# Kernel tuning notes

Measured on AMD Instinct MI355X. Metric: run time of the kernel, lower is better.

## Reference

```python
import jax, jax.numpy as jnp
import numpy as np

D = 1024
N = 16
H = D // N  # 64
F = 4096
LOG2E = 1.442695041


def _rms_norm(x, scale, eps=1e-6):
    var = jnp.mean(x * x, axis=-1, keepdims=True)
    return x * jax.lax.rsqrt(var + eps) * scale


def _layer_norm(x, gamma, beta, eps=1e-5):
    m = jnp.mean(x, axis=-1, keepdims=True)
    v = jnp.mean(jnp.square(x - m), axis=-1, keepdims=True)
    return (x - m) * jax.lax.rsqrt(v + eps) * gamma + beta


def setup_inputs() -> dict:
    key = jax.random.key(0)
    ks = jax.random.split(key, 12)
    B, T = 8, 1024
    s = 0.02
    return {
        "x": jax.random.normal(ks[0], (B, T, D), dtype=jnp.float32),
        "padding": jnp.ones((B, T), dtype=jnp.float32),
        "rms_scale": jnp.ones((D,), dtype=jnp.float32),
        "per_dim_scale": jnp.zeros((H,), dtype=jnp.float32),
        "wq": jax.random.normal(ks[1], (D, N, H), dtype=jnp.float32) * s,
        "bq": jnp.zeros((N, H), dtype=jnp.float32),
        "wk": jax.random.normal(ks[2], (D, N, H), dtype=jnp.float32) * s,
        "bk": jnp.zeros((N, H), dtype=jnp.float32),
        "wv": jax.random.normal(ks[3], (D, N, H), dtype=jnp.float32) * s,
        "bv": jnp.zeros((N, H), dtype=jnp.float32),
        "wo": jax.random.normal(ks[4], (D, N, H), dtype=jnp.float32) * s,
        "bo": jnp.zeros((D,), dtype=jnp.float32),
        "ln_gamma": jnp.ones((D,), dtype=jnp.float32),
        "ln_beta": jnp.zeros((D,), dtype=jnp.float32),
        "w1": jax.random.normal(ks[5], (D, F), dtype=jnp.float32) * s,
        "b1": jnp.zeros((F,), dtype=jnp.float32),
        "w2": jax.random.normal(ks[6], (F, D), dtype=jnp.float32) * s,
        "b2": jnp.zeros((D,), dtype=jnp.float32),
    }


def reference(x, padding, rms_scale, per_dim_scale, wq, bq, wk, bk, wv, bv,
              wo, bo, ln_gamma, ln_beta, w1, b1, w2, b2):
    B, T, _ = x.shape
    res = x
    # pre-norm (RMS) for attention block
    xn = _rms_norm(x, rms_scale)
    # causal + padding mask: [B, T, S]
    causal = jnp.tril(jnp.ones((T, T), dtype=x.dtype))
    mask = causal[None, :, :] * padding[:, :, None] * padding[:, None, :]
    # projections: [B,T,N,H]
    q = jnp.einsum("btd,dnh->btnh", xn, wq) + bq
    k = jnp.einsum("btd,dnh->btnh", xn, wk) + bk
    v = jnp.einsum("btd,dnh->btnh", xn, wv) + bv
    # per-dim scale: (log2(e)/sqrt(H)) * softplus(p)
    scale = (LOG2E / jnp.sqrt(jnp.asarray(H, x.dtype))) * jax.nn.softplus(per_dim_scale)
    q = q * scale
    # scores: [B,N,T,S]
    dot = jnp.einsum("btnh,bsnh->bnts", q, k)
    dot = jnp.where(mask[:, None, :, :] == 0, jnp.asarray(-1e9, dot.dtype), dot)
    attn_w = jax.nn.softmax(dot, axis=-1)
    attn_out = jnp.einsum("bnts,bsnh->btnh", attn_w, v)
    attn = jnp.einsum("btnh,dnh->btd", attn_out, wo) + bo
    attn = res + attn
    # FFN block (pre-norm LayerNorm)
    res2 = attn
    h = _layer_norm(attn, ln_gamma, ln_beta)
    h = jax.nn.relu(h @ w1 + b1)
    h = h @ w2 + b2
    return res2 + h
```

## Files before the change

kernel.cpp:

```cpp
#include <hip/hip_runtime.h>
#include <hip/hip_bf16.h>
#include <cstdint>
#include <cstddef>

#define BB    8
#define TT    1024
#define DD    1024
#define NHEAD 16
#define HDIM  64
#define FF    4096

typedef unsigned short u16;
typedef unsigned int   u32;
typedef short bf16x8 __attribute__((ext_vector_type(8)));
typedef float floatx4 __attribute__((ext_vector_type(4)));
typedef float floatx16 __attribute__((ext_vector_type(16)));
typedef __attribute__((address_space(1))) const u32 gu32;
typedef __attribute__((address_space(3))) u32 lu32;

#define ZERO16 {0.f,0.f,0.f,0.f,0.f,0.f,0.f,0.f,0.f,0.f,0.f,0.f,0.f,0.f,0.f,0.f}

__device__ __forceinline__ float b2f(u16 u) {
  union { u32 i; float f; } c; c.i = ((u32)u) << 16; return c.f;
}
__device__ __forceinline__ u16 f2b(float f) {
  union { float f; u32 i; } c; c.f = f;
  u32 x = c.i;
  u32 r = (x + 0x7fffu + ((x >> 16) & 1u)) >> 16;
  return (u16)r;
}

__global__ __launch_bounds__(256) void rms_kernel(const float* __restrict__ x,
                                                  const float* __restrict__ g,
                                                  u16* __restrict__ xn) {
  int row = blockIdx.x;
  int tid = threadIdx.x;
  float4 v = ((const float4*)(x + (size_t)row * DD))[tid];
  float ss = v.x*v.x + v.y*v.y + v.z*v.z + v.w*v.w;
  for (int off = 32; off; off >>= 1) ss += __shfl_xor(ss, off);
  __shared__ float red[4];
  if ((tid & 63) == 0) red[tid >> 6] = ss;
  __syncthreads();
  float tot = red[0] + red[1] + red[2] + red[3];
  float inv = rsqrtf(tot * (1.0f / DD) + 1e-6f);
  float4 gv = ((const float4*)g)[tid];
  ushort4 o;
  o.x = f2b(v.x * inv * gv.x);
  o.y = f2b(v.y * inv * gv.y);
  o.z = f2b(v.z * inv * gv.z);
  o.w = f2b(v.w * inv * gv.w);
  ((ushort4*)(xn + (size_t)row * DD))[tid] = o;
}

__global__ __launch_bounds__(256) void ln_kernel(const float* __restrict__ a,
                                                 const float* __restrict__ g,
                                                 const float* __restrict__ be,
                                                 u16* __restrict__ o) {
  int row = blockIdx.x;
  int tid = threadIdx.x;
  float4 v = ((const float4*)(a + (size_t)row * DD))[tid];
  float s1 = v.x + v.y + v.z + v.w;
  float s2 = v.x*v.x + v.y*v.y + v.z*v.z + v.w*v.w;
  for (int off = 32; off; off >>= 1) {
    s1 += __shfl_xor(s1, off);
    s2 += __shfl_xor(s2, off);
  }
  __shared__ float r1[4], r2[4];
  if ((tid & 63) == 0) { r1[tid >> 6] = s1; r2[tid >> 6] = s2; }
  __syncthreads();
  float S1 = r1[0] + r1[1] + r1[2] + r1[3];
  float S2 = r2[0] + r2[1] + r2[2] + r2[3];
  float mean = S1 * (1.0f / DD);
  float var  = S2 * (1.0f / DD) - mean * mean;
  float inv  = rsqrtf(var + 1e-5f);
  float4 gv = ((const float4*)g)[tid];
  float4 bv = ((const float4*)be)[tid];
  ushort4 out;
  out.x = f2b((v.x - mean) * inv * gv.x + bv.x);
  out.y = f2b((v.y - mean) * inv * gv.y + bv.y);
  out.z = f2b((v.z - mean) * inv * gv.z + bv.z);
  out.w = f2b((v.w - mean) * inv * gv.w + bv.w);
  ((ushort4*)(o + (size_t)row * DD))[tid] = out;
}

__global__ void prep_kernel(const float* __restrict__ bq, const float* __restrict__ bk,
                            const float* __restrict__ bv, const float* __restrict__ pds,
                            float* __restrict__ bqkv, float* __restrict__ qsall) {
  int j = blockIdx.x * 1024 + threadIdx.x;
  float b = (j < 1024) ? bq[j] : (j < 2048) ? bk[j - 1024] : bv[j - 2048];
  bqkv[j] = b;
  float s = 1.f;
  if (j < 1024) {
    float p = pds[j & 63];
    float sp = (p > 0.f) ? (p + log1pf(__expf(-p))) : log1pf(__expf(p));
    s = 0.26017112252f * sp;
  }
  qsall[j] = s;
}

__global__ __launch_bounds__(256) void transpose_conv(const float* __restrict__ in,
                                                      u16* __restrict__ out,
                                                      int R, int C) {
  __shared__ float t[32][33];
  int bx = blockIdx.x * 32, by = blockIdx.y * 32;
  int tx = threadIdx.x & 31, ty = threadIdx.x >> 5;
#pragma unroll
  for (int i = 0; i < 32; i += 8)
    t[ty + i][tx] = in[(size_t)(by + ty + i) * C + bx + tx];
  __syncthreads();
#pragma unroll
  for (int i = 0; i < 32; i += 8)
    out[(size_t)(bx + ty + i) * R + by + tx] = f2b(t[tx][ty + i]);
}

__global__ __launch_bounds__(256) void conv_bf16(const float* __restrict__ in,
                                                 u16* __restrict__ out) {
  int i = blockIdx.x * 256 + threadIdx.x;
  float4 v = ((const float4*)in)[i];
  ushort4 o = { f2b(v.x), f2b(v.y), f2b(v.z), f2b(v.w) };
  ((ushort4*)out)[i] = o;
}

__global__ __launch_bounds__(256) void vtrans_kernel(const u16* __restrict__ vsrc,
                                                     u16* __restrict__ vdst) {
  __shared__ u16 tile[64][65];
  int bn = blockIdx.y; int b = bn >> 4, n = bn & 15;
  int t0 = blockIdx.x * 64;
  int tid = threadIdx.x;
  int rr = tid >> 4;
  int c4 = (tid & 15) * 4;
#pragma unroll
  for (int i = 0; i < 4; i++) {
    int r = i * 16 + rr;
    ushort4 d = *(const ushort4*)(vsrc + ((size_t)(b * TT + t0 + r)) * DD + n * HDIM + c4);
    tile[r][c4 + 0] = d.x; tile[r][c4 + 1] = d.y;
    tile[r][c4 + 2] = d.z; tile[r][c4 + 3] = d.w;
  }
  __syncthreads();
#pragma unroll
  for (int i = 0; i < 4; i++) {
    int h = i * 16 + rr;
    ushort4 d;
    d.x = tile[c4 + 0][h]; d.y = tile[c4 + 1][h];
    d.z = tile[c4 + 2][h]; d.w = tile[c4 + 3][h];
    *(ushort4*)(vdst + ((size_t)bn * HDIM + h) * TT + t0 + c4) = d;
  }
}

template <typename OUT_T>
__global__ __launch_bounds__(256) void mfma_gemm(
    const u16* __restrict__ A, const u16* __restrict__ Bt,
    const float* __restrict__ bias, const float* __restrict__ accsrc,
    const float* __restrict__ scale, OUT_T* __restrict__ C,
    int lda, int ldb, int K, int relu, int ldc, size_t regstride) {
  __shared__ u16 As[128 * 32] __attribute__((aligned(16)));
  __shared__ u16 Bs[128 * 32] __attribute__((aligned(16)));
  int tid = threadIdx.x;
  int lane = tid & 63;
  int wave = tid >> 6;
  int nbx = gridDim.x;
  int nwg = nbx * gridDim.y;
  int bid = blockIdx.y * nbx + blockIdx.x;
  int wid = (bid & 7) * (nwg >> 3) + (bid >> 3);
  int row0 = (wid / nbx) * 128, col0 = (wid % nbx) * 128;

  int sr = tid >> 2;
  int sk = (tid & 3) << 3;
  const u16* ag = A  + (size_t)(row0 + sr) * lda + sk;
  const u16* bg = Bt + (size_t)(col0 + sr) * ldb + sk;
  u16* asl = As + tid * 8;
  u16* bsl = Bs + tid * 8;
  size_t rstepA = (size_t)64 * lda;
  size_t rstepB = (size_t)64 * ldb;

  int wr = (wave >> 1) * 64;
  int wc = (wave & 1) * 64;
  int fr = lane & 15;
  int fq = lane >> 4;

  const bf16x8* afp = (const bf16x8*)(As + (size_t)(wr + fr) * 32 + fq * 8);
  const bf16x8* bfp = (const bf16x8*)(Bs + (size_t)(wc + fr) * 32 + fq * 8);

  floatx4 acc[4][4];
#pragma unroll
  for (int mi = 0; mi < 4; mi++)
#pragma unroll
    for (int ni = 0; ni < 4; ni++)
      acc[mi][ni] = (floatx4){0.f, 0.f, 0.f, 0.f};

  for (int k0 = 0; k0 < K; k0 += 32) {
    __builtin_amdgcn_global_load_lds((gu32*)ag,            (lu32*)asl,          16, 0, 0);
    __builtin_amdgcn_global_load_lds((gu32*)(ag + rstepA), (lu32*)(asl + 2048), 16, 0, 0);
    __builtin_amdgcn_global_load_lds((gu32*)bg,            (lu32*)bsl,          16, 0, 0);
    __builtin_amdgcn_global_load_lds((gu32*)(bg + rstepB), (lu32*)(bsl + 2048), 16, 0, 0);
    __syncthreads();
    bf16x8 af[4], bf[4];
#pragma unroll
    for (int mi = 0; mi < 4; mi++) af[mi] = afp[mi * 64];
#pragma unroll
    for (int ni = 0; ni < 4; ni++) bf[ni] = bfp[ni * 64];
#pragma unroll
    for (int mi = 0; mi < 4; mi++)
#pragma unroll
      for (int ni = 0; ni < 4; ni++)
        acc[mi][ni] = __builtin_amdgcn_mfma_f32_16x16x32_bf16(
            af[mi], bf[ni], acc[mi][ni], 0, 0, 0);
    __syncthreads();
    ag += 32; bg += 32;
  }

#pragma unroll
  for (int mi = 0; mi < 4; mi++) {
    int rbase = row0 + wr + mi * 16 + fq * 4;
#pragma unroll
    for (int ni = 0; ni < 4; ni++) {
      int col = col0 + wc + ni * 16 + fr;
      float bcol = bias ? bias[col] : 0.f;
      float scl  = scale ? scale[col] : 1.f;
      size_t cbase = regstride ? ((size_t)(col >> 10) * regstride + (col & 1023))
                               : (size_t)col;
#pragma unroll
      for (int reg = 0; reg < 4; reg++) {
        int r = rbase + reg;
        float v = (acc[mi][ni][reg] + bcol) * scl;
        if (relu)   v = fmaxf(v, 0.f);
        if (accsrc) v += accsrc[(size_t)r * ldc + col];
        if constexpr (sizeof(OUT_T) == 2) ((u16*)C)[cbase + (size_t)r * ldc] = f2b(v);
        else                              ((float*)C)[cbase + (size_t)r * ldc] = v;
      }
    }
  }
}

__global__ __launch_bounds__(256) void attn_mfma(
    const u16* __restrict__ q, const u16* __restrict__ k,
    const u16* __restrict__ vT, const float* __restrict__ padc,
    u16* __restrict__ ao) {
  int nwg = gridDim.x * gridDim.y;
  int bid = blockIdx.y * gridDim.x + blockIdx.x;
  int wid = (bid & 7) * (nwg >> 3) + (bid >> 3);
  int p  = wid & 3;
  int bn = wid >> 2;
  int b = bn >> 4, n = bn & 15;
  int tid = threadIdx.x;
  int w = tid >> 6, lane = tid & 63;
  int cl = lane & 31, hf = lane >> 5;
  __shared__ u16 Qs[128 * 64] __attribute__((aligned(16)));
  __shared__ u16 Ks[64 * 64]  __attribute__((aligned(16)));
  __shared__ u16 Vts[64 * 64] __attribute__((aligned(16)));
  __shared__ float padl[64];

  for (int half = 0; half < 2; half++) {
    int qt = half ? (7 - p) : p;
    int q0g = qt * 128;

#pragma unroll
    for (int it = 0; it < 4; it++) {
      int cid = it * 256 + tid; int r = cid >> 3, cc = cid & 7;
      uint4 d = *(const uint4*)(q + ((size_t)(b * TT + q0g + r)) * DD + n * HDIM + cc * 8);
      ((uint4*)Qs)[r * 8 + (cc ^ (r & 7))] = d;
    }
    __syncthreads();
    bf16x8 qf[4];
    int qrow = 32 * w + cl;
#pragma unroll
    for (int kc = 0; kc < 4; kc++)
      qf[kc] = ((const bf16x8*)Qs)[qrow * 8 + ((2 * kc + hf) ^ (cl & 7))];

    int tq = q0g + qrow;
    float prow = padc[b * TT + tq];
    bool prow_ok = (prow != 0.f);
    floatx16 o0 = ZERO16, o1 = ZERO16;
    float m_i = -INFINITY, l_i = 0.f;

    int jend = q0g + 128;
    for (int j0 = 0; j0 < jend; j0 += 64) {
#pragma unroll
      for (int it = 0; it < 2; it++) {
        int cid = it * 256 + tid; int r = cid >> 3, cc = cid & 7;
        uint4 dk = *(const uint4*)(k + ((size_t)(b * TT + j0 + r)) * DD + n * HDIM + cc * 8);
        ((uint4*)Ks)[r * 8 + (cc ^ (r & 7))] = dk;
        uint4 dv = *(const uint4*)(vT + ((size_t)(bn * HDIM + r)) * TT + j0 + cc * 8);
        ((uint4*)Vts)[r * 8 + (cc ^ (r & 7))] = dv;
      }
      if (tid < 64) padl[tid] = padc[b * TT + j0 + tid];
      __syncthreads();

      floatx16 s0 = ZERO16, s1 = ZERO16;
#pragma unroll
      for (int kc = 0; kc < 4; kc++) {
        bf16x8 ka0 = ((const bf16x8*)Ks)[cl * 8 + ((2 * kc + hf) ^ (cl & 7))];
        bf16x8 ka1 = ((const bf16x8*)Ks)[(32 + cl) * 8 + ((2 * kc + hf) ^ (cl & 7))];
        s0 = __builtin_amdgcn_mfma_f32_32x32x16_bf16(ka0, qf[kc], s0, 0, 0, 0);
        s1 = __builtin_amdgcn_mfma_f32_32x32x16_bf16(ka1, qf[kc], s1, 0, 0, 0);
      }

      float pl = padl[lane];
      bool fullt = (j0 + 63 <= q0g + 32 * w) && __all(pl != 0.f) && __all((int)prow_ok);
      float mloc = -INFINITY;
      if (fullt) {
#pragma unroll
        for (int i = 0; i < 16; i++)
          mloc = fmaxf(mloc, fmaxf(s0[i], s1[i]));
      } else {
#pragma unroll
        for (int q2 = 0; q2 < 2; q2++) {
#pragma unroll
          for (int rg = 0; rg < 4; rg++) {
            float4 pv = *(const float4*)&padl[q2 * 32 + rg * 8 + 4 * hf];
            int kb = j0 + q2 * 32 + rg * 8 + 4 * hf;
#pragma unroll
            for (int j = 0; j < 4; j++) {
              int idx = rg * 4 + j;
              float sval = q2 ? s1[idx] : s0[idx];
              float pvj = (j == 0) ? pv.x : (j == 1) ? pv.y : (j == 2) ? pv.z : pv.w;
              bool ok = prow_ok && (kb + j <= tq) && (pvj != 0.f);
              sval = ok ? sval : -1e9f;
              if (q2) s1[idx] = sval; else s0[idx] = sval;
              mloc = fmaxf(mloc, sval);
            }
          }
        }
      }
      float mtile = fmaxf(mloc, __shfl_xor(mloc, 32));
      float mnew = fmaxf(m_i, mtile);
      float alpha = exp2f(m_i - mnew);
      m_i = mnew;
      float ls = 0.f;
#pragma unroll
      for (int i = 0; i < 16; i++) {
        float p0 = exp2f(s0[i] - mnew); s0[i] = p0; ls += p0;
        float p1 = exp2f(s1[i] - mnew); s1[i] = p1; ls += p1;
      }
      ls += __shfl_xor(ls, 32);
      l_i = l_i * alpha + ls;
      o0 *= alpha; o1 *= alpha;

      u32 pk[8][2];
#pragma unroll
      for (int q2 = 0; q2 < 2; q2++)
#pragma unroll
        for (int rg = 0; rg < 4; rg++) {
          int be = q2 * 4 + rg;
          float a0 = q2 ? s1[rg * 4 + 0] : s0[rg * 4 + 0];
          float a1 = q2 ? s1[rg * 4 + 1] : s0[rg * 4 + 1];
          float a2 = q2 ? s1[rg * 4 + 2] : s0[rg * 4 + 2];
          float a3 = q2 ? s1[rg * 4 + 3] : s0[rg * 4 + 3];
          pk[be][0] = (u32)f2b(a0) | ((u32)f2b(a1) << 16);
          pk[be][1] = (u32)f2b(a2) | ((u32)f2b(a3) << 16);
        }
      u32 pp[8][2];
#pragma unroll
      for (int be = 0; be < 8; be++) {
        pp[be][0] = (u32)__shfl_xor((int)pk[be][0], 32);
        pp[be][1] = (u32)__shfl_xor((int)pk[be][1], 32);
      }

#pragma unroll
      for (int kc = 0; kc < 4; kc++) {
        union { u32 wd[4]; bf16x8 v; } pb;
        if (hf == 0) {
          pb.wd[0] = pk[2 * kc][0];     pb.wd[1] = pk[2 * kc][1];
          pb.wd[2] = pp[2 * kc][0];     pb.wd[3] = pp[2 * kc][1];
        } else {
          pb.wd[0] = pp[2 * kc + 1][0]; pb.wd[1] = pp[2 * kc + 1][1];
          pb.wd[2] = pk[2 * kc + 1][0]; pb.wd[3] = pk[2 * kc + 1][1];
        }
        bf16x8 vf0 = ((const bf16x8*)Vts)[cl * 8 + ((2 * kc + hf) ^ (cl & 7))];
        bf16x8 vf1 = ((const bf16x8*)Vts)[(32 + cl) * 8 + ((2 * kc + hf) ^ (cl & 7))];
        o0 = __builtin_amdgcn_mfma_f32_32x32x16_bf16(vf0, pb.v, o0, 0, 0, 0);
        o1 = __builtin_amdgcn_mfma_f32_32x32x16_bf16(vf1, pb.v, o1, 0, 0, 0);
      }
      __syncthreads();
    }

    float rl = 1.f / l_i;
#pragma unroll
    for (int hq = 0; hq < 2; hq++)
#pragma unroll
      for (int rg = 0; rg < 4; rg++) {
        ushort4 st;
        st.x = f2b((hq ? o1[rg * 4 + 0] : o0[rg * 4 + 0]) * rl);
        st.y = f2b((hq ? o1[rg * 4 + 1] : o0[rg * 4 + 1]) * rl);
        st.z = f2b((hq ? o1[rg * 4 + 2] : o0[rg * 4 + 2]) * rl);
        st.w = f2b((hq ? o1[rg * 4 + 3] : o0[rg * 4 + 3]) * rl);
        int col = n * HDIM + hq * 32 + rg * 8 + 4 * hf;
        *(ushort4*)(ao + ((size_t)(b * TT + tq)) * DD + col) = st;
      }
  }
}

extern "C" void kernel_launch(void* const* d_in, const int* in_sizes, int n_in,
                              void* d_out, int out_size, void* d_ws, size_t ws_size,
                              hipStream_t stream) {
  const float* x   = (const float*)d_in[0];
  const float* pad = (const float*)d_in[1];
  const float* rs  = (const float*)d_in[2];
  const float* pds = (const float*)d_in[3];
  const float* wq  = (const float*)d_in[4];
  const float* bq  = (const float*)d_in[5];
  const float* wk  = (const float*)d_in[6];
  const float* bk  = (const float*)d_in[7];
  const float* wv_ = (const float*)d_in[8];
  const float* bv  = (const float*)d_in[9];
  const float* wo  = (const float*)d_in[10];
  const float* bo  = (const float*)d_in[11];
  const float* lg  = (const float*)d_in[12];
  const float* lb  = (const float*)d_in[13];
  const float* w1  = (const float*)d_in[14];
  const float* b1  = (const float*)d_in[15];
  const float* w2  = (const float*)d_in[16];
  const float* b2  = (const float*)d_in[17];
  float* out = (float*)d_out;

  const size_t MB = (size_t)1 << 20;
  int G;
  if      (ws_size >= 88 * MB) G = 8;
  else if (ws_size >= 56 * MB) G = 4;
  else if (ws_size >= 40 * MB) G = 2;
  else                         G = 1;

  char* w = (char*)d_ws;
  u16* wqkvT = (u16*)(w);
  u16* woT   = (u16*)(w + 6 * MB);
  u16* w1T   = (u16*)(w + 8 * MB);
  u16* w2T   = (u16*)(w + 16 * MB);
  char* act = w + 24 * MB;
  const size_t SA = (size_t)2 * G * MB;
  u16*   regA = (u16*)act;
  u16*   qB   = (u16*)(act + SA);
  u16*   kC   = (u16*)(act + 2 * SA);
  u16*   vD   = (u16*)(act + 3 * SA);
  u16*   vTr  = regA;
  u16*   ao   = vD;
  u16*   hn   = regA;
  u16*   h1h  = qB;

  float* bqkv  = out + (size_t)out_size - 8192;
  float* qsall = bqkv + 3072;

  transpose_conv<<<dim3(32, 32),  256, 0, stream>>>(wq,  wqkvT,              DD, DD);
  transpose_conv<<<dim3(32, 32),  256, 0, stream>>>(wk,  wqkvT + 1024 * 1024, DD, DD);
  transpose_conv<<<dim3(32, 32),  256, 0, stream>>>(wv_, wqkvT + 2048 * 1024, DD, DD);
  conv_bf16<<<1024, 256, 0, stream>>>(wo, woT);
  transpose_conv<<<dim3(128, 32), 256, 0, stream>>>(w1, w1T, DD, FF);
  transpose_conv<<<dim3(32, 128), 256, 0, stream>>>(w2, w2T, FF, DD);
  prep_kernel<<<3, 1024, 0, stream>>>(bq, bk, bv, pds, bqkv, qsall);

  const int R = G * 1024;

  for (int c0 = 0; c0 < BB / G; c0++) {
    size_t rowoff = (size_t)c0 * R;
    const float* xc = x + rowoff * DD;
    float* outc = out + rowoff * DD;

    rms_kernel<<<R, 256, 0, stream>>>(xc, rs, regA);

    mfma_gemm<u16><<<dim3(24, R / 128), 256, 0, stream>>>(
        regA, wqkvT, bqkv, nullptr, qsall, qB,
        DD, DD, DD, 0, 1024, (size_t)R * 1024);

    vtrans_kernel<<<dim3(TT / 64, G * NHEAD), 256, 0, stream>>>(vD, vTr);

    attn_mfma<<<dim3(4, G * NHEAD), 256, 0, stream>>>(
        qB, kC, vTr, pad + rowoff, ao);

    mfma_gemm<float><<<dim3(8, R / 128), 256, 0, stream>>>(
        ao, woT, bo, xc, nullptr, outc, DD, DD, DD, 0, 1024, 0);

    ln_kernel<<<R, 256, 0, stream>>>(outc, lg, lb, hn);

    for (int f = 0; f < 2; f++) {
      mfma_gemm<u16><<<dim3(16, R / 128), 256, 0, stream>>>(
          hn, w1T + (size_t)f * 2048 * 1024, b1 + f * 2048, nullptr, nullptr,
          h1h, DD, DD, DD, 1, 2048, 0);
      mfma_gemm<float><<<dim3(8, R / 128), 256, 0, stream>>>(
          h1h, w2T + f * 2048, (f == 0) ? b2 : nullptr, outc, nullptr,
          outc, 2048, FF, 2048, 0, 1024, 0);
    }
  }
}
```

Measured before the change: 632.4 us.

## Add 256x256-tile, 512-thread GEMM with 4-stage LDS pipeline for all projections

```diff
diff --git a/kernel.cpp b/kernel.cpp
--- a/kernel.cpp
+++ b/kernel.cpp
@@ -144,6 +144,118 @@
     d.x = tile[c4 + 0][h]; d.y = tile[c4 + 1][h];
     d.z = tile[c4 + 2][h]; d.w = tile[c4 + 3][h];
     *(ushort4*)(vdst + ((size_t)bn * HDIM + h) * TT + t0 + c4) = d;
+  }
+}
+
+template <typename OUT_T>
+__global__ __launch_bounds__(512, 2) void mfma_gemm256(
+    const u16* __restrict__ A, const u16* __restrict__ Bt,
+    const float* __restrict__ bias, const float* __restrict__ accsrc,
+    const float* __restrict__ scale, OUT_T* __restrict__ C,
+    int lda, int ldb, int K, int relu, int ldc, size_t regstride) {
+  __shared__ u16 AS[4][256 * 32] __attribute__((aligned(16)));
+  __shared__ u16 BS[4][256 * 32] __attribute__((aligned(16)));
+  int tid = threadIdx.x;
+  int lane = tid & 63;
+  int wv = tid >> 6;
+  int nbx = gridDim.x;
+  int nwg = nbx * gridDim.y;
+  int bid = blockIdx.y * nbx + blockIdx.x;
+  int wid = (bid & 7) * (nwg >> 3) + (bid >> 3);
+  int row0 = (wid / nbx) * 256, col0 = (wid % nbx) * 256;
+
+  int sr = tid >> 2;
+  int sk = (tid & 3) << 3;
+  const u16* ag = A  + (size_t)(row0 + sr) * lda + sk;
+  const u16* bg = Bt + (size_t)(col0 + sr) * ldb + sk;
+  size_t rstepA = (size_t)128 * lda;
+  size_t rstepB = (size_t)128 * ldb;
+
+  int fr = lane & 15, fq = lane >> 4;
+  int wr = (wv >> 2) * 128;
+  int wc = (wv & 3) * 64;
+
+  floatx4 acc[8][4];
+#pragma unroll
+  for (int mi = 0; mi < 8; mi++)
+#pragma unroll
+    for (int ni = 0; ni < 4; ni++)
+      acc[mi][ni] = (floatx4){0.f, 0.f, 0.f, 0.f};
+
+#define STAGE_A(tt)                                                            \
+  { u16* d_ = AS[(tt) & 3] + tid * 8; const u16* g_ = ag + (tt) * 32;          \
+    __builtin_amdgcn_global_load_lds((gu32*)g_, (lu32*)d_, 16, 0, 0);          \
+    __builtin_amdgcn_global_load_lds((gu32*)(g_ + rstepA), (lu32*)(d_ + 4096), 16, 0, 0); }
+#define STAGE_B(tt)                                                            \
+  { u16* d_ = BS[(tt) & 3] + tid * 8; const u16* g_ = bg + (tt) * 32;          \
+    __builtin_amdgcn_global_load_lds((gu32*)g_, (lu32*)d_, 16, 0, 0);          \
+    __builtin_amdgcn_global_load_lds((gu32*)(g_ + rstepB), (lu32*)(d_ + 4096), 16, 0, 0); }
+#define GBAR() asm volatile("s_barrier" ::: "memory")
+#define PHASE(s, q, ...)                                                       \
+  { const u16* As_ = AS[s]; const u16* Bs_ = BS[s];                            \
+    bf16x8 af[4], bf[4];                                                       \
+    _Pragma("unroll")                                                          \
+    for (int mi = 0; mi < 4; mi++)                                             \
+      af[mi] = *(const bf16x8*)(As_ + (size_t)(wr + (q) * 64 + mi * 16 + fr) * 32 + fq * 8); \
+    _Pragma("unroll")                                                          \
+    for (int ni = 0; ni < 4; ni++)                                             \
+      bf[ni] = *(const bf16x8*)(Bs_ + (size_t)(wc + ni * 16 + fr) * 32 + fq * 8); \
+    __VA_ARGS__;                                                               \
+    __builtin_amdgcn_s_setprio(1);                                             \
+    _Pragma("unroll")                                                          \
+    for (int mi = 0; mi < 4; mi++)                                             \
+      _Pragma("unroll")                                                        \
+      for (int ni = 0; ni < 4; ni++)                                           \
+        acc[(q) * 4 + mi][ni] = __builtin_amdgcn_mfma_f32_16x16x32_bf16(       \
+            af[mi], bf[ni], acc[(q) * 4 + mi][ni], 0, 0, 0);                   \
+    __builtin_amdgcn_s_setprio(0); }
+
+  int NT = K >> 5;
+  STAGE_A(0) STAGE_B(0) STAGE_A(1) STAGE_B(1) STAGE_A(2) STAGE_B(2)
+
+  for (int t = 0; t < NT - 3; ++t) {
+    int s = t & 3;
+    asm volatile("s_waitcnt vmcnt(8)" ::: "memory");
+    GBAR();
+    PHASE(s, 0, STAGE_A(t + 3))
+    GBAR();
+    PHASE(s, 1, STAGE_B(t + 3))
+  }
+  { int s = (NT - 3) & 3;
+    asm volatile("s_waitcnt vmcnt(8)" ::: "memory");
+    GBAR(); PHASE(s, 0, ) GBAR(); PHASE(s, 1, ) }
+  { int s = (NT - 2) & 3;
+    asm volatile("s_waitcnt vmcnt(4)" ::: "memory");
+    GBAR(); PHASE(s, 0, ) GBAR(); PHASE(s, 1, ) }
+  { int s = (NT - 1) & 3;
+    asm volatile("s_waitcnt vmcnt(0)" ::: "memory");
+    GBAR(); PHASE(s, 0, ) GBAR(); PHASE(s, 1, ) }
+
+#undef PHASE
+#undef GBAR
+#undef STAGE_A
+#undef STAGE_B
+
+#pragma unroll
+  for (int mi = 0; mi < 8; mi++) {
+    int rbase = row0 + wr + mi * 16 + fq * 4;
+#pragma unroll
+    for (int ni = 0; ni < 4; ni++) {
+      int col = col0 + wc + ni * 16 + fr;
+      float bcol = bias ? bias[col] : 0.f;
+      float scl  = scale ? scale[col] : 1.f;
+      size_t cbase = regstride ? ((size_t)(col >> 10) * regstride + (col & 1023))
+                               : (size_t)col;
+#pragma unroll
+      for (int reg = 0; reg < 4; reg++) {
+        int r = rbase + reg;
+        float v = (acc[mi][ni][reg] + bcol) * scl;
+        if (relu)   v = fmaxf(v, 0.f);
+        if (accsrc) v += accsrc[(size_t)r * ldc + col];
+        if constexpr (sizeof(OUT_T) == 2) ((u16*)C)[cbase + (size_t)r * ldc] = f2b(v);
+        else                              ((float*)C)[cbase + (size_t)r * ldc] = v;
+      }
+    }
   }
 }
 
@@ -456,7 +568,7 @@
 
     rms_kernel<<<R, 256, 0, stream>>>(xc, rs, regA);
 
-    mfma_gemm<u16><<<dim3(24, R / 128), 256, 0, stream>>>(
+    mfma_gemm256<u16><<<dim3(12, R / 256), 512, 0, stream>>>(
         regA, wqkvT, bqkv, nullptr, qsall, qB,
         DD, DD, DD, 0, 1024, (size_t)R * 1024);
 
@@ -465,16 +577,16 @@
     attn_mfma<<<dim3(4, G * NHEAD), 256, 0, stream>>>(
         qB, kC, vTr, pad + rowoff, ao);
 
-    mfma_gemm<float><<<dim3(8, R / 128), 256, 0, stream>>>(
+    mfma_gemm256<float><<<dim3(4, R / 256), 512, 0, stream>>>(
         ao, woT, bo, xc, nullptr, outc, DD, DD, DD, 0, 1024, 0);
 
     ln_kernel<<<R, 256, 0, stream>>>(outc, lg, lb, hn);
 
     for (int f = 0; f < 2; f++) {
-      mfma_gemm<u16><<<dim3(16, R / 128), 256, 0, stream>>>(
+      mfma_gemm256<u16><<<dim3(8, R / 256), 512, 0, stream>>>(
           hn, w1T + (size_t)f * 2048 * 1024, b1 + f * 2048, nullptr, nullptr,
           h1h, DD, DD, DD, 1, 2048, 0);
-      mfma_gemm<float><<<dim3(8, R / 128), 256, 0, stream>>>(
+      mfma_gemm256<float><<<dim3(4, R / 256), 512, 0, stream>>>(
           h1h, w2T + f * 2048, (f == 0) ? b2 : nullptr, outc, nullptr,
           outc, 2048, FF, 2048, 0, 1024, 0);
     }
```

Measured after the change: 712.4 us. 1.13x slower.

## Triple-buffer GEMM LDS tiles with async global_load_lds prefetch two stages ahead

Applied to the files above, without the earlier changes.

```diff
diff --git a/kernel.cpp b/kernel.cpp
--- a/kernel.cpp
+++ b/kernel.cpp
@@ -153,8 +153,8 @@
     const float* __restrict__ bias, const float* __restrict__ accsrc,
     const float* __restrict__ scale, OUT_T* __restrict__ C,
     int lda, int ldb, int K, int relu, int ldc, size_t regstride) {
-  __shared__ u16 As[128 * 32] __attribute__((aligned(16)));
-  __shared__ u16 Bs[128 * 32] __attribute__((aligned(16)));
+  __shared__ u16 As[3][128 * 32] __attribute__((aligned(16)));
+  __shared__ u16 Bs[3][128 * 32] __attribute__((aligned(16)));
   int tid = threadIdx.x;
   int lane = tid & 63;
   int wave = tid >> 6;
@@ -168,8 +168,6 @@
   int sk = (tid & 3) << 3;
   const u16* ag = A  + (size_t)(row0 + sr) * lda + sk;
   const u16* bg = Bt + (size_t)(col0 + sr) * ldb + sk;
-  u16* asl = As + tid * 8;
-  u16* bsl = Bs + tid * 8;
   size_t rstepA = (size_t)64 * lda;
   size_t rstepB = (size_t)64 * ldb;
 
@@ -178,9 +176,6 @@
   int fr = lane & 15;
   int fq = lane >> 4;
 
-  const bf16x8* afp = (const bf16x8*)(As + (size_t)(wr + fr) * 32 + fq * 8);
-  const bf16x8* bfp = (const bf16x8*)(Bs + (size_t)(wc + fr) * 32 + fq * 8);
-
   floatx4 acc[4][4];
 #pragma unroll
   for (int mi = 0; mi < 4; mi++)
@@ -188,12 +183,29 @@
     for (int ni = 0; ni < 4; ni++)
       acc[mi][ni] = (floatx4){0.f, 0.f, 0.f, 0.f};
 
-  for (int k0 = 0; k0 < K; k0 += 32) {
-    __builtin_amdgcn_global_load_lds((gu32*)ag,            (lu32*)asl,          16, 0, 0);
-    __builtin_amdgcn_global_load_lds((gu32*)(ag + rstepA), (lu32*)(asl + 2048), 16, 0, 0);
-    __builtin_amdgcn_global_load_lds((gu32*)bg,            (lu32*)bsl,          16, 0, 0);
-    __builtin_amdgcn_global_load_lds((gu32*)(bg + rstepB), (lu32*)(bsl + 2048), 16, 0, 0);
-    __syncthreads();
+#define STAGE(tt)                                                              \
+  { int s_ = (tt) % 3;                                                         \
+    u16* asl = As[s_] + tid * 8;                                               \
+    u16* bsl = Bs[s_] + tid * 8;                                               \
+    const u16* a_ = ag + (size_t)(tt) * 32;                                    \
+    const u16* b_ = bg + (size_t)(tt) * 32;                                    \
+    __builtin_amdgcn_global_load_lds((gu32*)a_,            (lu32*)asl,          16, 0, 0); \
+    __builtin_amdgcn_global_load_lds((gu32*)(a_ + rstepA), (lu32*)(asl + 2048), 16, 0, 0); \
+    __builtin_amdgcn_global_load_lds((gu32*)b_,            (lu32*)bsl,          16, 0, 0); \
+    __builtin_amdgcn_global_load_lds((gu32*)(b_ + rstepB), (lu32*)(bsl + 2048), 16, 0, 0); }
+
+  int NT = K >> 5;
+  STAGE(0)
+  STAGE(1)
+
+  for (int t = 0; t < NT; ++t) {
+    if (t < NT - 1) asm volatile("s_waitcnt vmcnt(4)" ::: "memory");
+    else            asm volatile("s_waitcnt vmcnt(0)" ::: "memory");
+    asm volatile("s_barrier" ::: "memory");
+    if (t + 2 < NT) STAGE(t + 2)
+    int s = t % 3;
+    const bf16x8* afp = (const bf16x8*)(As[s] + (size_t)(wr + fr) * 32 + fq * 8);
+    const bf16x8* bfp = (const bf16x8*)(Bs[s] + (size_t)(wc + fr) * 32 + fq * 8);
     bf16x8 af[4], bf[4];
 #pragma unroll
     for (int mi = 0; mi < 4; mi++) af[mi] = afp[mi * 64];
@@ -205,9 +217,8 @@
       for (int ni = 0; ni < 4; ni++)
         acc[mi][ni] = __builtin_amdgcn_mfma_f32_16x16x32_bf16(
             af[mi], bf[ni], acc[mi][ni], 0, 0, 0);
-    __syncthreads();
-    ag += 32; bg += 32;
-  }
+  }
+#undef STAGE
 
 #pragma unroll
   for (int mi = 0; mi < 4; mi++) {
```

Result: faster. 602.5 us (-4.7%).
